# Kernel tuning notes

Hardware: AMD Instinct MI355X
Metric: run time of the kernel (lower is better)

The kernel has to match this reference:

```python
import jax, jax.numpy as jnp
import numpy as np

N = 100_000        # num nodes
E = 1_600_000      # num edges (avg degree 16)
F_IN = 128         # input node feature dim
F_E = 32           # edge feature dim
D = 32             # out_dim per head
H = 4              # heads


def setup_inputs() -> dict:
    key = jax.random.key(0)
    ks = jax.random.split(key, 8)
    s = 0.05
    return {
        "node_features": jax.random.normal(ks[0], (N, F_IN), jnp.float32),
        "edge_index": jax.random.randint(ks[1], (E, 2), 0, N, jnp.int32),
        "edge_features": jax.random.normal(ks[2], (E, F_E), jnp.float32),
        "W_node": jax.random.normal(ks[3], (F_IN, D * H), jnp.float32) * s,
        "W_edge": jax.random.normal(ks[4], (F_E, D * H), jnp.float32) * s,
        "attn_kernel": jax.random.normal(ks[5], (H, 3 * D), jnp.float32) * s,
        "W_out": jax.random.normal(ks[6], (D * H, D), jnp.float32) * s,
        "b_out": jnp.zeros((D,), jnp.float32),
    }


def segment_softmax(logits, seg, num_segments):
    # logits: [E, H], seg: [E] destination node ids
    mx = jax.ops.segment_max(logits, seg, num_segments=num_segments)   # [N, H]
    ex = jnp.exp(logits - mx[seg])
    denom = jax.ops.segment_sum(ex, seg, num_segments=num_segments)    # [N, H]
    return ex / (denom[seg] + 1e-8)


def reference(node_features, edge_index, edge_features, W_node, W_edge,
              attn_kernel, W_out, b_out):
    src_idx = edge_index[:, 0]
    dst_idx = edge_index[:, 1]

    # Node / edge projections -> [*, H, D]
    node_proj = (node_features @ W_node).reshape(N, H, D)
    edge_proj = (edge_features @ W_edge).reshape(E, H, D)

    # attn_kernel is [H, 3D] applied to concat(src, dst, edge); split it so we
    # never materialize the [E, H, 3D] concat. Src/dst terms are computed
    # per-node then gathered (same math, far less traffic).
    a_src, a_dst, a_edge = attn_kernel[:, :D], attn_kernel[:, D:2 * D], attn_kernel[:, 2 * D:]
    s_src = jnp.einsum('nhd,hd->nh', node_proj, a_src)   # [N, H]
    s_dst = jnp.einsum('nhd,hd->nh', node_proj, a_dst)   # [N, H]
    s_edge = jnp.einsum('ehd,hd->eh', edge_proj, a_edge)  # [E, H]

    logits = s_src[src_idx] + s_dst[dst_idx] + s_edge     # [E, H]
    attn = segment_softmax(logits, dst_idx, N)             # [E, H]

    src_feat = node_proj[src_idx]                          # [E, H, D]
    messages = (attn[:, :, None] * src_feat).reshape(E, H * D)
    agg = jax.ops.segment_sum(messages, dst_idx, num_segments=N)  # [N, H*D]

    out = jax.nn.gelu(agg @ W_out + b_out, approximate=False)     # exact erf GELU
    return out
```

## Files before the change

### kernel.cpp

```cpp
#include <hip/hip_runtime.h>
#include <hip/hip_bf16.h>
#include <hip/hip_fp16.h>

#define F_IN 128
#define F_E  32
#define DH   128
#define HD   32

__device__ __forceinline__ unsigned short f2bf(float f) {
    unsigned int x = __float_as_uint(f);
    unsigned int r = (x + 0x7fffu + ((x >> 16) & 1u)) >> 16;
    return (unsigned short)r;
}

__global__ void prep_kernel(const float* __restrict__ W_edge,
                            const float* __restrict__ attn,
                            float* __restrict__ wefold) {
    int t = threadIdx.x;
    int f = t >> 2, h = t & 3;
    float s = 0.f;
#pragma unroll
    for (int d = 0; d < 32; ++d)
        s += W_edge[f * DH + h * HD + d] * attn[h * 96 + 64 + d];
    wefold[f * 4 + h] = s;
}

__global__ __launch_bounds__(256, 4)
void node_proj_kernel(const float* __restrict__ x, const float* __restrict__ Wn,
                      const float* __restrict__ attn,
                      unsigned short* __restrict__ proj_bf,
                      float* __restrict__ s_src, int N) {
    __shared__ float xsT[32 * 132];
    __shared__ float ws[32 * 132];
    const int t  = threadIdx.x;
    const int n0 = blockIdx.x * 128;
    const int tc = t & 15, tn = t >> 4;
    const float4* x4  = (const float4*)x;
    const float4* Wn4 = (const float4*)Wn;

    float acc[2][2][4][4];
#pragma unroll
    for (int a = 0; a < 2; ++a)
#pragma unroll
        for (int b = 0; b < 2; ++b)
#pragma unroll
            for (int i = 0; i < 4; ++i)
#pragma unroll
                for (int j = 0; j < 4; ++j) acc[a][b][i][j] = 0.f;

    for (int ch = 0; ch < 4; ++ch) {
        __syncthreads();
#pragma unroll
        for (int j = 0; j < 4; ++j) {
            int idx = t + j * 256;
            int n  = idx >> 3;
            int kq = idx & 7;
            float4 v = make_float4(0.f, 0.f, 0.f, 0.f);
            if (n0 + n < N) v = x4[(size_t)(n0 + n) * 32 + ch * 8 + kq];
            int kk = kq * 4;
            xsT[(kk + 0) * 132 + n] = v.x;
            xsT[(kk + 1) * 132 + n] = v.y;
            xsT[(kk + 2) * 132 + n] = v.z;
            xsT[(kk + 3) * 132 + n] = v.w;
        }
#pragma unroll
        for (int j = 0; j < 4; ++j) {
            int idx = t + j * 256;
            int kk = idx >> 5, cq = idx & 31;
            float4 v = Wn4[(size_t)(ch * 32 + kk) * 32 + cq];
            *(float4*)&ws[kk * 132 + cq * 4] = v;
        }
        __syncthreads();
#pragma unroll 4
        for (int kk = 0; kk < 32; ++kk) {
            float4 a0 = *(const float4*)&xsT[kk * 132 + tn * 4];
            float4 a1 = *(const float4*)&xsT[kk * 132 + 64 + tn * 4];
            float4 b0 = *(const float4*)&ws[kk * 132 + tc * 4];
            float4 b1 = *(const float4*)&ws[kk * 132 + 64 + tc * 4];
            float av[2][4] = {{a0.x, a0.y, a0.z, a0.w}, {a1.x, a1.y, a1.z, a1.w}};
            float bv[2][4] = {{b0.x, b0.y, b0.z, b0.w}, {b1.x, b1.y, b1.z, b1.w}};
#pragma unroll
            for (int ni = 0; ni < 2; ++ni)
#pragma unroll
                for (int ci = 0; ci < 2; ++ci)
#pragma unroll
                    for (int ii = 0; ii < 4; ++ii)
#pragma unroll
                        for (int jj = 0; jj < 4; ++jj)
                            acc[ni][ci][ii][jj] =
                                fmaf(av[ni][ii], bv[ci][jj], acc[ni][ci][ii][jj]);
        }
    }

    float asv[2][4];
#pragma unroll
    for (int ci = 0; ci < 2; ++ci)
#pragma unroll
        for (int jj = 0; jj < 4; ++jj) {
            int c = ci * 64 + tc * 4 + jj;
            int h = c >> 5, d = c & 31;
            asv[ci][jj] = attn[h * 96 + d];
        }

#pragma unroll
    for (int ni = 0; ni < 2; ++ni)
#pragma unroll
        for (int ii = 0; ii < 4; ++ii) {
            int n = n0 + ni * 64 + tn * 4 + ii;
            bool ok = (n < N);
            if (ok) {
                union { unsigned short h[4]; uint2 u; } p0, p1;
#pragma unroll
                for (int jj = 0; jj < 4; ++jj) {
                    p0.h[jj] = f2bf(acc[ni][0][ii][jj]);
                    p1.h[jj] = f2bf(acc[ni][1][ii][jj]);
                }
                *(uint2*)&proj_bf[(size_t)n * DH + tc * 4]      = p0.u;
                *(uint2*)&proj_bf[(size_t)n * DH + 64 + tc * 4] = p1.u;
            }
#pragma unroll
            for (int ci = 0; ci < 2; ++ci) {
                float ps = 0.f;
#pragma unroll
                for (int jj = 0; jj < 4; ++jj)
                    ps = fmaf(acc[ni][ci][ii][jj], asv[ci][jj], ps);
                ps += __shfl_xor(ps, 1);
                ps += __shfl_xor(ps, 2);
                ps += __shfl_xor(ps, 4);
                if (ok && (tc & 7) == 0) {
                    int h = ci * 2 + (tc >> 3);
                    s_src[n * 4 + h] = ps;
                }
            }
        }
}

__global__ __launch_bounds__(256)
void edgeprep_kernel(const float* __restrict__ ef, const int* __restrict__ eidx,
                     const float* __restrict__ wefold,
                     const float* __restrict__ s_src,
                     int* __restrict__ cnt, uint4* __restrict__ rec_e, int E) {
    __shared__ float wf[128];
    const int t = threadIdx.x;
    if (t < 128) wf[t] = wefold[t];
    __syncthreads();

    const int e = blockIdx.x * 256 + t;
    if (e >= E) return;
    int2 sd = ((const int2*)eidx)[e];
    int s_i = sd.x, d_i = sd.y;
    float es0 = 0.f, es1 = 0.f, es2 = 0.f, es3 = 0.f;
#pragma unroll
    for (int f4 = 0; f4 < 8; ++f4) {
        float4 v = *(const float4*)&ef[(size_t)e * F_E + f4 * 4];
        float vv[4] = {v.x, v.y, v.z, v.w};
#pragma unroll
        for (int q = 0; q < 4; ++q) {
            float4 wv = *(const float4*)&wf[(f4 * 4 + q) * 4];
            es0 = fmaf(vv[q], wv.x, es0);
            es1 = fmaf(vv[q], wv.y, es1);
            es2 = fmaf(vv[q], wv.z, es2);
            es3 = fmaf(vv[q], wv.w, es3);
        }
    }
    float4 a = *(const float4*)&s_src[s_i * 4];
    float w0 = __expf(a.x + es0), w1 = __expf(a.y + es1);
    float w2 = __expf(a.z + es2), w3 = __expf(a.w + es3);
    unsigned int u0 = __half_as_ushort(__float2half_rn(w0));
    unsigned int u1 = __half_as_ushort(__float2half_rn(w1));
    unsigned int u2 = __half_as_ushort(__float2half_rn(w2));
    unsigned int u3 = __half_as_ushort(__float2half_rn(w3));
    int r = atomicAdd(&cnt[d_i], 1);
    uint4 R;
    R.x = (unsigned int)s_i;
    R.y = u0 | (u1 << 16);
    R.z = u2 | (u3 << 16);
    R.w = ((unsigned int)d_i << 15) | (unsigned int)r;
    rec_e[e] = R;
}

__global__ __launch_bounds__(256)
void scan1_kernel(const int* __restrict__ cnt, int* __restrict__ cursor,
                  int* __restrict__ bsum, int N) {
    __shared__ int s[256];
    const int t = threadIdx.x;
    int i = blockIdx.x * 256 + t;
    int v = (i < N) ? cnt[i] : 0;
    s[t] = v;
    __syncthreads();
#pragma unroll
    for (int d = 1; d < 256; d <<= 1) {
        int x = (t >= d) ? s[t - d] : 0;
        __syncthreads();
        s[t] += x;
        __syncthreads();
    }
    if (i < N) cursor[i] = s[t] - v;
    if (t == 255) bsum[blockIdx.x] = s[255];
}

__global__ __launch_bounds__(512)
void scan2_kernel(int* __restrict__ bsum, int nb) {
    __shared__ int s[512];
    const int t = threadIdx.x;
    int v = (t < nb) ? bsum[t] : 0;
    s[t] = v;
    __syncthreads();
#pragma unroll
    for (int d = 1; d < 512; d <<= 1) {
        int x = (t >= d) ? s[t - d] : 0;
        __syncthreads();
        s[t] += x;
        __syncthreads();
    }
    if (t < nb) bsum[t] = s[t] - v;
}

__global__ __launch_bounds__(256)
void scan3_kernel(int* __restrict__ cursor, const int* __restrict__ bsum, int N) {
    int i = blockIdx.x * 256 + threadIdx.x;
    if (i < N) cursor[i] += bsum[blockIdx.x];
}

__global__ __launch_bounds__(256)
void scatter_kernel(const uint4* __restrict__ rec_e,
                    const int* __restrict__ cursor,
                    uint4* __restrict__ rec, int E) {
    const int e = blockIdx.x * 256 + threadIdx.x;
    if (e >= E) return;
    uint4 R = rec_e[e];
    int d = (int)(R.w >> 15);
    int r = (int)(R.w & 32767u);
    int pos = cursor[d] + r;
    rec[pos] = R;
}

__global__ __launch_bounds__(256)
void gather_kernel(const int* __restrict__ cursor, const uint4* __restrict__ rec,
                   const unsigned int* __restrict__ proj_bf,
                   unsigned int* __restrict__ numer_bf, int N, int E) {
    const int t    = threadIdx.x;
    const int lane = t & 63;
    const int n    = blockIdx.x * 4 + (t >> 6);
    if (n >= N) return;

    const int start = cursor[n];
    const int end   = (n == N - 1) ? E : cursor[n + 1];
    const int h     = lane >> 4;

    float2 acc = make_float2(0.f, 0.f);
    float dsum = 0.f;

    int i = start;
    for (; i + 4 <= end; i += 4) {
        uint4 r[4];
#pragma unroll
        for (int q = 0; q < 4; ++q) r[q] = rec[i + q];
        unsigned int pv[4];
#pragma unroll
        for (int q = 0; q < 4; ++q)
            pv[q] = proj_bf[(size_t)r[q].x * 64 + lane];
#pragma unroll
        for (int q = 0; q < 4; ++q) {
            unsigned int packed = (h < 2) ? r[q].y : r[q].z;
            unsigned short uw = (h & 1) ? (unsigned short)(packed >> 16)
                                        : (unsigned short)(packed & 0xffffu);
            float w = __half2float(__ushort_as_half(uw));
            dsum += w;
            acc.x = fmaf(w, __uint_as_float(pv[q] << 16), acc.x);
            acc.y = fmaf(w, __uint_as_float(pv[q] & 0xffff0000u), acc.y);
        }
    }
    for (; i < end; ++i) {
        uint4 r = rec[i];
        unsigned int u = proj_bf[(size_t)r.x * 64 + lane];
        unsigned int packed = (h < 2) ? r.y : r.z;
        unsigned short uw = (h & 1) ? (unsigned short)(packed >> 16)
                                    : (unsigned short)(packed & 0xffffu);
        float w = __half2float(__ushort_as_half(uw));
        dsum += w;
        acc.x = fmaf(w, __uint_as_float(u << 16), acc.x);
        acc.y = fmaf(w, __uint_as_float(u & 0xffff0000u), acc.y);
    }

    float r = 1.f / (dsum + 1e-8f);
    unsigned int p = (unsigned int)f2bf(acc.x * r) |
                     ((unsigned int)f2bf(acc.y * r) << 16);
    numer_bf[(size_t)n * 64 + lane] = p;
}

__global__ __launch_bounds__(256, 2)
void out_kernel(const unsigned int* __restrict__ numer_bf,
                const float* __restrict__ Wout, const float* __restrict__ bout,
                float* __restrict__ out, int N) {
    __shared__ float wsh[128 * 32];
    __shared__ float bsh[32];
    const int t = threadIdx.x;
    for (int i = t; i < 4096; i += 256) wsh[i] = Wout[i];
    if (t < 32) bsh[t] = bout[t];
    __syncthreads();

    int n = blockIdx.x * 256 + t;
    if (n >= N) return;

    float acc[32];
#pragma unroll
    for (int j = 0; j < 32; ++j) acc[j] = 0.f;

    for (int kg = 0; kg < 16; ++kg) {
        uint4 v = *(const uint4*)&numer_bf[(size_t)n * 64 + kg * 4];
        unsigned int vv[4] = {v.x, v.y, v.z, v.w};
#pragma unroll
        for (int q = 0; q < 4; ++q) {
            int k = kg * 8 + q * 2;
            float a0 = __uint_as_float(vv[q] << 16);
            float a1 = __uint_as_float(vv[q] & 0xffff0000u);
#pragma unroll
            for (int j = 0; j < 32; j += 4) {
                float4 w0 = *(const float4*)&wsh[k * 32 + j];
                float4 w1 = *(const float4*)&wsh[(k + 1) * 32 + j];
                acc[j + 0] = fmaf(a0, w0.x, fmaf(a1, w1.x, acc[j + 0]));
                acc[j + 1] = fmaf(a0, w0.y, fmaf(a1, w1.y, acc[j + 1]));
                acc[j + 2] = fmaf(a0, w0.z, fmaf(a1, w1.z, acc[j + 2]));
                acc[j + 3] = fmaf(a0, w0.w, fmaf(a1, w1.w, acc[j + 3]));
            }
        }
    }
#pragma unroll
    for (int j = 0; j < 32; ++j) {
        float z = acc[j] + bsh[j];
        acc[j] = 0.5f * z * (1.f + erff(z * 0.70710678118654752f));
    }
#pragma unroll
    for (int j = 0; j < 32; j += 4)
        *(float4*)&out[(size_t)n * 32 + j] = make_float4(acc[j], acc[j+1], acc[j+2], acc[j+3]);
}

extern "C" void kernel_launch(void* const* d_in, const int* in_sizes, int n_in,
                              void* d_out, int out_size, void* d_ws, size_t ws_size,
                              hipStream_t stream) {
    const float* x    = (const float*)d_in[0];
    const int*   eidx = (const int*)d_in[1];
    const float* ef   = (const float*)d_in[2];
    const float* Wn   = (const float*)d_in[3];
    const float* We   = (const float*)d_in[4];
    const float* attn = (const float*)d_in[5];
    const float* Wout = (const float*)d_in[6];
    const float* bout = (const float*)d_in[7];
    float* out = (float*)d_out;

    const int N = in_sizes[0] / F_IN;
    const int E = in_sizes[1] / 2;
    const int NB = (N + 255) / 256;

    char* ws = (char*)d_ws;
    size_t off = 0;
    auto alloc = [&](size_t bytes) {
        void* p = ws + off;
        off = (off + bytes + 255) & ~(size_t)255;
        return p;
    };
    int*   cnt     = (int*)  alloc((size_t)N * 4);
    size_t zero_bytes = off;
    int*   cursor  = (int*)  alloc((size_t)N * 4);
    int*   bsum    = (int*)  alloc(512 * 4);
    float* wefold  = (float*)alloc(512);
    float* s_src   = (float*)alloc((size_t)N * 4 * 4);
    unsigned short* proj_bf = (unsigned short*)alloc((size_t)N * DH * 2);
    size_t numer_bytes = (size_t)N * 64 * 4;
    size_t rece_bytes  = (size_t)E * 16;
    unsigned int* numer_bf = (unsigned int*)alloc(numer_bytes > rece_bytes ?
                                                  numer_bytes : rece_bytes);
    uint4* rec_e   = (uint4*)numer_bf;
    uint4* rec     = (uint4*)alloc((size_t)E * 16);

    hipMemsetAsync(d_ws, 0, zero_bytes, stream);
    hipLaunchKernelGGL(prep_kernel, dim3(1), dim3(128), 0, stream, We, attn, wefold);
    hipLaunchKernelGGL(node_proj_kernel, dim3((N + 127) / 128), dim3(256), 0, stream,
                       x, Wn, attn, proj_bf, s_src, N);
    hipLaunchKernelGGL(edgeprep_kernel, dim3((E + 255) / 256), dim3(256), 0, stream,
                       ef, eidx, wefold, s_src, cnt, rec_e, E);
    hipLaunchKernelGGL(scan1_kernel, dim3(NB), dim3(256), 0, stream, cnt, cursor, bsum, N);
    hipLaunchKernelGGL(scan2_kernel, dim3(1), dim3(512), 0, stream, bsum, NB);
    hipLaunchKernelGGL(scan3_kernel, dim3(NB), dim3(256), 0, stream, cursor, bsum, N);
    hipLaunchKernelGGL(scatter_kernel, dim3((E + 255) / 256), dim3(256), 0, stream,
                       rec_e, cursor, rec, E);
    hipLaunchKernelGGL(gather_kernel, dim3((N + 3) / 4), dim3(256), 0, stream,
                       cursor, rec, (const unsigned int*)proj_bf, numer_bf, N, E);
    hipLaunchKernelGGL(out_kernel, dim3((N + 255) / 256), dim3(256), 0, stream,
                       numer_bf, Wout, bout, out, N);
}
```

Measured before the change: 546.4 us.

## Fold scan block offsets into consumers and software-pipeline gather edge record loads

Removes the scan3 kernel launch by adding the per-block prefix offset from bsum directly in the scatter and gather kernels. The gather loop is restructured to double-buffer the edge records: it prefetches the next group of four records while the current group's feature loads and FMAs run. Tail edges are handled by masking, with index 0 and zero weight standing in for absent edges, instead of a scalar remainder loop. Segment bounds are made wave-uniform with readfirstlane, and the rec buffer is padded so the over-reads stay in bounds. The cost is an extra bsum load per edge and per node, plus some wasted loads on short segments.

After: 528.4 us. 1.03x faster.

```diff
diff --git a/kernel.cpp b/kernel.cpp
--- a/kernel.cpp
+++ b/kernel.cpp
@@ -217,26 +217,22 @@
 }
 
 __global__ __launch_bounds__(256)
-void scan3_kernel(int* __restrict__ cursor, const int* __restrict__ bsum, int N) {
-    int i = blockIdx.x * 256 + threadIdx.x;
-    if (i < N) cursor[i] += bsum[blockIdx.x];
-}
-
-__global__ __launch_bounds__(256)
 void scatter_kernel(const uint4* __restrict__ rec_e,
                     const int* __restrict__ cursor,
+                    const int* __restrict__ bsum,
                     uint4* __restrict__ rec, int E) {
     const int e = blockIdx.x * 256 + threadIdx.x;
     if (e >= E) return;
     uint4 R = rec_e[e];
     int d = (int)(R.w >> 15);
     int r = (int)(R.w & 32767u);
-    int pos = cursor[d] + r;
+    int pos = cursor[d] + bsum[d >> 8] + r;
     rec[pos] = R;
 }
 
 __global__ __launch_bounds__(256)
-void gather_kernel(const int* __restrict__ cursor, const uint4* __restrict__ rec,
+void gather_kernel(const int* __restrict__ cursor, const int* __restrict__ bsum,
+                   const uint4* __restrict__ rec,
                    const unsigned int* __restrict__ proj_bf,
                    unsigned int* __restrict__ numer_bf, int N, int E) {
     const int t    = threadIdx.x;
@@ -244,25 +240,39 @@
     const int n    = blockIdx.x * 4 + (t >> 6);
     if (n >= N) return;
 
-    const int start = cursor[n];
-    const int end   = (n == N - 1) ? E : cursor[n + 1];
-    const int h     = lane >> 4;
+    int start = cursor[n] + bsum[n >> 8];
+    int end   = (n == N - 1) ? E : (cursor[n + 1] + bsum[(n + 1) >> 8]);
+    start = __builtin_amdgcn_readfirstlane(start);
+    end   = __builtin_amdgcn_readfirstlane(end);
+    const int h = lane >> 4;
 
     float2 acc = make_float2(0.f, 0.f);
     float dsum = 0.f;
 
-    int i = start;
-    for (; i + 4 <= end; i += 4) {
-        uint4 r[4];
-#pragma unroll
-        for (int q = 0; q < 4; ++q) r[q] = rec[i + q];
+    int i   = start;
+    int rem = end - start;
+    int c0  = rem < 4 ? rem : 4;
+    uint4 ra[4];
+#pragma unroll
+    for (int q = 0; q < 4; ++q) ra[q] = rec[i + q];
+
+    while (c0 > 0) {
+        const int i1   = i + c0;
+        const int rem1 = rem - c0;
+        const int c1   = rem1 < 4 ? rem1 : 4;
+        uint4 rb[4];
+#pragma unroll
+        for (int q = 0; q < 4; ++q) rb[q] = rec[i1 + q];
         unsigned int pv[4];
 #pragma unroll
-        for (int q = 0; q < 4; ++q)
-            pv[q] = proj_bf[(size_t)r[q].x * 64 + lane];
-#pragma unroll
         for (int q = 0; q < 4; ++q) {
-            unsigned int packed = (h < 2) ? r[q].y : r[q].z;
+            unsigned int s = (q < c0) ? ra[q].x : 0u;
+            pv[q] = proj_bf[(size_t)s * 64 + lane];
+        }
+#pragma unroll
+        for (int q = 0; q < 4; ++q) {
+            unsigned int packed = (h < 2) ? ra[q].y : ra[q].z;
+            packed = (q < c0) ? packed : 0u;
             unsigned short uw = (h & 1) ? (unsigned short)(packed >> 16)
                                         : (unsigned short)(packed & 0xffffu);
             float w = __half2float(__ushort_as_half(uw));
@@ -270,17 +280,9 @@
             acc.x = fmaf(w, __uint_as_float(pv[q] << 16), acc.x);
             acc.y = fmaf(w, __uint_as_float(pv[q] & 0xffff0000u), acc.y);
         }
-    }
-    for (; i < end; ++i) {
-        uint4 r = rec[i];
-        unsigned int u = proj_bf[(size_t)r.x * 64 + lane];
-        unsigned int packed = (h < 2) ? r.y : r.z;
-        unsigned short uw = (h & 1) ? (unsigned short)(packed >> 16)
-                                    : (unsigned short)(packed & 0xffffu);
-        float w = __half2float(__ushort_as_half(uw));
-        dsum += w;
-        acc.x = fmaf(w, __uint_as_float(u << 16), acc.x);
-        acc.y = fmaf(w, __uint_as_float(u & 0xffff0000u), acc.y);
+#pragma unroll
+        for (int q = 0; q < 4; ++q) ra[q] = rb[q];
+        i = i1; rem = rem1; c0 = c1;
     }
 
     float r = 1.f / (dsum + 1e-8f);
@@ -372,7 +374,7 @@
     unsigned int* numer_bf = (unsigned int*)alloc(numer_bytes > rece_bytes ?
                                                   numer_bytes : rece_bytes);
     uint4* rec_e   = (uint4*)numer_bf;
-    uint4* rec     = (uint4*)alloc((size_t)E * 16);
+    uint4* rec     = (uint4*)alloc((size_t)E * 16 + 64);
 
     hipMemsetAsync(d_ws, 0, zero_bytes, stream);
     hipLaunchKernelGGL(prep_kernel, dim3(1), dim3(128), 0, stream, We, attn, wefold);
@@ -382,11 +384,10 @@
                        ef, eidx, wefold, s_src, cnt, rec_e, E);
     hipLaunchKernelGGL(scan1_kernel, dim3(NB), dim3(256), 0, stream, cnt, cursor, bsum, N);
     hipLaunchKernelGGL(scan2_kernel, dim3(1), dim3(512), 0, stream, bsum, NB);
-    hipLaunchKernelGGL(scan3_kernel, dim3(NB), dim3(256), 0, stream, cursor, bsum, N);
     hipLaunchKernelGGL(scatter_kernel, dim3((E + 255) / 256), dim3(256), 0, stream,
-                       rec_e, cursor, rec, E);
+                       rec_e, cursor, bsum, rec, E);
     hipLaunchKernelGGL(gather_kernel, dim3((N + 3) / 4), dim3(256), 0, stream,
-                       cursor, rec, (const unsigned int*)proj_bf, numer_bf, N, E);
+                       cursor, bsum, rec, (const unsigned int*)proj_bf, numer_bf, N, E);
     hipLaunchKernelGGL(out_kernel, dim3((N + 255) / 256), dim3(256), 0, stream,
                        numer_bf, Wout, bout, out, N);
 }
```
